# Performance work log

Measured on AMD Instinct MI355X. Metric: run time of the kernel, lower is better.

The kernel has to match this reference:

```python
import jax, jax.numpy as jnp
import numpy as np

NUM_EXPERTS = 4


def _conv1x1(w, b, x):
    # w: [out,in], b: [out], x: [B,in,H,W]
    return jnp.einsum('oc,bchw->bohw', w, x) + b[None, :, None, None]


def _sobel(x):
    c = x.shape[1]
    kx = jnp.array([[-1., 0., 1.], [-2., 0., 2.], [-1., 0., 1.]], dtype=x.dtype)
    ky = jnp.array([[-1., -2., -1.], [0., 0., 0.], [1., 2., 1.]], dtype=x.dtype)
    wx = jnp.broadcast_to(kx[None, None], (c, 1, 3, 3))
    wy = jnp.broadcast_to(ky[None, None], (c, 1, 3, 3))
    dn = ('NCHW', 'OIHW', 'NCHW')
    gx = jax.lax.conv_general_dilated(x, wx, (1, 1), [(1, 1), (1, 1)],
                                      dimension_numbers=dn, feature_group_count=c)
    gy = jax.lax.conv_general_dilated(x, wy, (1, 1), [(1, 1), (1, 1)],
                                      dimension_numbers=dn, feature_group_count=c)
    return gx, gy


def _bilinear_sample(x, gx, gy):
    # torch F.grid_sample(mode='bilinear', padding_mode='zeros', align_corners=False)
    # x: [B,C,H,W]; gx, gy: [B,Hs,Ws] normalized coords in [-1,1]
    B, C, H, W = x.shape
    ix = ((gx + 1.0) * W - 1.0) * 0.5
    iy = ((gy + 1.0) * H - 1.0) * 0.5
    x0 = jnp.floor(ix)
    y0 = jnp.floor(iy)
    wx1 = ix - x0
    wx0 = 1.0 - wx1
    wy1 = iy - y0
    wy0 = 1.0 - wy1
    xf = x.reshape(B, C, H * W)

    def gather(xc, yc):
        valid = (xc >= 0) & (xc <= W - 1) & (yc >= 0) & (yc <= H - 1)
        xi = jnp.clip(xc, 0, W - 1).astype(jnp.int32)
        yi = jnp.clip(yc, 0, H - 1).astype(jnp.int32)
        idx = yi * W + xi  # [B,Hs,Ws]
        v = jax.vmap(lambda xb, ib: xb[:, ib])(xf, idx)  # [B,C,Hs,Ws]
        return v * valid[:, None].astype(x.dtype)

    return (gather(x0, y0) * (wx0 * wy0)[:, None]
            + gather(x0 + 1, y0) * (wx1 * wy0)[:, None]
            + gather(x0, y0 + 1) * (wx0 * wy1)[:, None]
            + gather(x0 + 1, y0 + 1) * (wx1 * wy1)[:, None])


def _forward(x, wc_e, we_e, wb1, bb1, wb2, bb2, wr, br, wo, bo, wcv, bcv, scale, scale2):
    B, c, h, w = x.shape
    sh = round(h * scale)
    sw = round(w * scale2)

    grad_x, grad_y = _sobel(x)

    # relative-offset coordinate embedding, [1,4,sh,sw]
    ih = (jnp.arange(sh, dtype=x.dtype) + 0.5) / scale
    coor_h = ih - jnp.floor(ih + 0.001) - 0.5  # [sh]
    iw = (jnp.arange(sw, dtype=x.dtype) + 0.5) / scale2
    coor_w = iw - jnp.floor(iw + 0.001) - 0.5  # [sw]
    inp = jnp.stack([
        jnp.full((sh, sw), 1.0 / scale2, dtype=x.dtype),
        jnp.full((sh, sw), 1.0 / scale, dtype=x.dtype),
        jnp.broadcast_to(coor_h[:, None], (sh, sw)),
        jnp.broadcast_to(coor_w[None, :], (sh, sw)),
    ], axis=0)[None]

    emb = jax.nn.relu(_conv1x1(wb2, bb2, jax.nn.relu(_conv1x1(wb1, bb1, inp))))
    offset = _conv1x1(wo, bo, emb)                 # [1,2,sh,sw]
    routing = jax.nn.sigmoid(_conv1x1(wr, br, emb))  # [1,E,sh,sw]

    # per-pixel soft mixture of expert compress/expand matrices
    rw = routing.reshape(NUM_EXPERTS, sh * sw).T   # [N,E]
    wc = (rw @ wc_e.reshape(NUM_EXPERTS, -1)).reshape(sh, sw, c // 8, c)
    we = (rw @ we_e.reshape(NUM_EXPERTS, -1)).reshape(sh, sw, c, c // 8)

    feat = _conv1x1(wcv, bcv, jnp.concatenate([x, grad_x, grad_y], axis=1))  # [B,64,h,w]

    # base grid (align_corners=True-style normalization, as in the source) + learned offsets
    gx0 = ((jnp.arange(sw, dtype=x.dtype) + 0.5) / scale2 - 0.5) * 2.0 / (w - 1) - 1.0
    gy0 = ((jnp.arange(sh, dtype=x.dtype) + 0.5) / scale - 0.5) * 2.0 / (h - 1) - 1.0
    gx = jnp.broadcast_to(gx0[None, None, :] + offset[:, 0] * (2.0 / (w - 1)), (B, sh, sw))
    gy = jnp.broadcast_to(gy0[None, :, None] + offset[:, 1] * (2.0 / (h - 1)), (B, sh, sw))

    fea0 = _bilinear_sample(feat, gx, gy)          # [B,64,sh,sw]

    mid = jnp.einsum('hwkc,bchw->bhwk', wc, fea0)  # per-pixel compress (k=C//8)
    out = jnp.einsum('hwck,bhwk->bchw', we, mid)   # per-pixel expand
    return out + fea0


def setup_inputs() -> dict:
    key = jax.random.key(0)
    ks = jax.random.split(key, 13)
    s = 0.05
    return {
        'x': jax.random.normal(ks[0], (2, 64, 192, 192), jnp.float32),
        'weight_compress': jax.random.normal(ks[1], (4, 8, 64), jnp.float32) * s,
        'weight_expand': jax.random.normal(ks[2], (4, 64, 8), jnp.float32) * s,
        'w_body1': jax.random.normal(ks[3], (64, 4), jnp.float32) * s,
        'b_body1': jax.random.normal(ks[4], (64,), jnp.float32) * s,
        'w_body2': jax.random.normal(ks[5], (64, 64), jnp.float32) * s,
        'b_body2': jax.random.normal(ks[6], (64,), jnp.float32) * s,
        'w_routing': jax.random.normal(ks[7], (4, 64), jnp.float32) * s,
        'b_routing': jax.random.normal(ks[8], (4,), jnp.float32) * s,
        'w_offset': jax.random.normal(ks[9], (2, 64), jnp.float32) * s,
        'b_offset': jax.random.normal(ks[10], (2,), jnp.float32) * s,
        'w_conv': jax.random.normal(ks[11], (64, 192), jnp.float32) * s,
        'b_conv': jax.random.normal(ks[12], (64,), jnp.float32) * s,
        'scale': 2,
        'scale2': 2,
    }


def reference(x, weight_compress, weight_expand, w_body1, b_body1, w_body2, b_body2,
              w_routing, b_routing, w_offset, b_offset, w_conv, b_conv, scale, scale2):
    return _forward(x, weight_compress, weight_expand, w_body1, b_body1, w_body2, b_body2,
                    w_routing, b_routing, w_offset, b_offset, w_conv, b_conv, scale, scale2)
```

## Files before the change

### kernel.cpp

```cpp
#include <hip/hip_runtime.h>
#include <hip/hip_bf16.h>
#include <math.h>

#define BN  2
#define CN  64
#define HN  192
#define WN  192
#define SH  384
#define SW  384
#define HW  (HN * WN)
#define NPIX (BN * HN * WN)

typedef __attribute__((ext_vector_type(8))) short bf16x8;
typedef __attribute__((ext_vector_type(4))) float f32x4;

#define KPAD 200

__device__ inline unsigned short f2bf(float f) {
    unsigned int u = __float_as_uint(f);
    u += 0x7fffu + ((u >> 16) & 1u);
    return (unsigned short)(u >> 16);
}

__device__ inline void sobel_col(const float* __restrict__ xc,
    size_t oT, size_t oM, size_t oB, int j, int jL, int jR,
    float mt, float mb, float mLt, float mLm, float mLb,
    float mRt, float mRm, float mRb, bool isL, bool isR,
    float& m_out, float& sx, float& sy)
{
    float t   = xc[oT + j] * mt;
    float m   = xc[oM + j];
    float btm = xc[oB + j] * mb;
    float hLt = xc[oT + jL] * mLt;
    float hLm = xc[oM + jL] * mLm;
    float hLb = xc[oB + jL] * mLb;
    float hRt = xc[oT + jR] * mRt;
    float hRm = xc[oM + jR] * mRm;
    float hRb = xc[oB + jR] * mRb;
    float tl  = __shfl_up(t, 1),   ml_ = __shfl_up(m, 1),   bl_ = __shfl_up(btm, 1);
    float tr  = __shfl_down(t, 1), mr_ = __shfl_down(m, 1), br_ = __shfl_down(btm, 1);
    float n0 = isL ? hLt : tl;
    float n3 = isL ? hLm : ml_;
    float n6 = isL ? hLb : bl_;
    float n2 = isR ? hRt : tr;
    float n5 = isR ? hRm : mr_;
    float n8 = isR ? hRb : br_;
    m_out = m;
    sx = (n2 - n0) + 2.f * (n5 - n3) + (n8 - n6);
    sy = (n6 - n0) + 2.f * (btm - t) + (n8 - n2);
}

__global__ __launch_bounds__(256) void feat_kernel(
    const float* __restrict__ x,
    const float* __restrict__ wcv,
    const float* __restrict__ bcv,
    float* __restrict__ feat)
{
    __shared__ unsigned short Bs[64 * KPAD];

    int bi = blockIdx.x;
    int jt = bi % 3;
    int t2 = bi / 3;
    int i  = t2 % HN;
    int b  = t2 / HN;
    int j0 = jt * 64;

    int tid  = threadIdx.x;
    int w    = __builtin_amdgcn_readfirstlane(tid >> 6);
    int lane = tid & 63;

    int mrow = (w << 4) + (lane & 15);
    int kb   = (lane >> 4) << 3;
    bf16x8 afrag[6];
    {
        const float* wr_ = wcv + mrow * 192 + kb;
#pragma unroll
        for (int ks = 0; ks < 6; ++ks) {
            float4 lo = *(const float4*)(wr_ + ks * 32);
            float4 hi = *(const float4*)(wr_ + ks * 32 + 4);
            bf16x8 a;
            a[0] = (short)f2bf(lo.x); a[1] = (short)f2bf(lo.y);
            a[2] = (short)f2bf(lo.z); a[3] = (short)f2bf(lo.w);
            a[4] = (short)f2bf(hi.x); a[5] = (short)f2bf(hi.y);
            a[6] = (short)f2bf(hi.z); a[7] = (short)f2bf(hi.w);
            afrag[ks] = a;
        }
    }

    bool ok_t = (i > 0), ok_b = (i < HN - 1);
    bool okL = (j0 > 0), okR = (j0 + 64 < WN);
    float mt = ok_t ? 1.f : 0.f, mb = ok_b ? 1.f : 0.f;
    int rT = ok_t ? i - 1 : i;
    int rB = ok_b ? i + 1 : i;
    int jL = okL ? j0 - 1 : j0;
    int jR = okR ? j0 + 64 : j0;
    float mLt = okL ? mt : 0.f, mLm = okL ? 1.f : 0.f, mLb = okL ? mb : 0.f;
    float mRt = okR ? mt : 0.f, mRm = okR ? 1.f : 0.f, mRb = okR ? mb : 0.f;
    bool isL = (lane == 0), isR = (lane == 63);

    const float* xb = x + (size_t)b * CN * HW;
    size_t oT = (size_t)rT * WN, oM = (size_t)i * WN, oB = (size_t)rB * WN;
    int j = j0 + lane;

    unsigned short* brow = Bs + lane * KPAD;
#pragma unroll 2
    for (int cp = 0; cp < 8; ++cp) {
        int c0 = (w << 4) + (cp << 1);
        float m0, sx0, sy0, m1, sx1, sy1;
        sobel_col(xb + (size_t)c0 * HW, oT, oM, oB, j, jL, jR,
                  mt, mb, mLt, mLm, mLb, mRt, mRm, mRb, isL, isR, m0, sx0, sy0);
        sobel_col(xb + (size_t)(c0 + 1) * HW, oT, oM, oB, j, jL, jR,
                  mt, mb, mLt, mLm, mLb, mRt, mRm, mRb, isL, isR, m1, sx1, sy1);
        *(unsigned int*)(brow + c0)       = (unsigned int)f2bf(m0)  | ((unsigned int)f2bf(m1)  << 16);
        *(unsigned int*)(brow + 64 + c0)  = (unsigned int)f2bf(sx0) | ((unsigned int)f2bf(sx1) << 16);
        *(unsigned int*)(brow + 128 + c0) = (unsigned int)f2bf(sy0) | ((unsigned int)f2bf(sy1) << 16);
    }

    __syncthreads();

    f32x4 acc[4] = {};
    const unsigned short* bp = Bs + (lane & 15) * KPAD + ((lane >> 4) << 3);
#pragma unroll
    for (int nt = 0; nt < 4; ++nt) {
        const unsigned short* bnt = bp + nt * 16 * KPAD;
#pragma unroll
        for (int ks = 0; ks < 6; ++ks) {
            bf16x8 bf = *(const bf16x8*)(bnt + ks * 32);
            acc[nt] = __builtin_amdgcn_mfma_f32_16x16x32_bf16(afrag[ks], bf, acc[nt], 0, 0, 0);
        }
    }

    int n0 = j0 + (lane & 15);
    int mbase = (w << 4) + ((lane >> 4) << 2);
    size_t outb = (size_t)b * CN * HW + (size_t)i * WN;
#pragma unroll
    for (int rr = 0; rr < 4; ++rr) {
        int m = mbase + rr;
        float bias = bcv[m];
        size_t rowb = outb + (size_t)m * HW + n0;
#pragma unroll
        for (int nt = 0; nt < 4; ++nt)
            feat[rowb + nt * 16] = acc[nt][rr] + bias;
    }
}

__device__ inline void run_mlp(int lane, float in0, float in1, float chv, float cwv,
    const float* __restrict__ wb1, const float* __restrict__ bb1,
    const float* __restrict__ wb2, const float* __restrict__ bb2,
    const float* __restrict__ wr,  const float* __restrict__ wo, float p[6])
{
    float4 w1 = ((const float4*)wb1)[lane];
    float h1 = fmaxf(bb1[lane] + w1.x * in0 + w1.y * in1 + w1.z * chv + w1.w * cwv, 0.f);
    const float4* w2row = (const float4*)(wb2 + lane * 64);
    float acc = bb2[lane];
#pragma unroll
    for (int q = 0; q < 16; ++q) {
        float4 wv = w2row[q];
        acc += wv.x * __shfl(h1, q * 4 + 0)
             + wv.y * __shfl(h1, q * 4 + 1)
             + wv.z * __shfl(h1, q * 4 + 2)
             + wv.w * __shfl(h1, q * 4 + 3);
    }
    float h2 = fmaxf(acc, 0.f);
#pragma unroll
    for (int e = 0; e < 4; ++e) p[e] = wr[e * 64 + lane] * h2;
#pragma unroll
    for (int e = 0; e < 2; ++e) p[4 + e] = wo[e * 64 + lane] * h2;
#pragma unroll
    for (int m = 1; m < 64; m <<= 1) {
#pragma unroll
        for (int e = 0; e < 6; ++e) p[e] += __shfl_xor(p[e], m);
    }
}

__global__ __launch_bounds__(256) void mlp_table_kernel(
    const float* __restrict__ wb1, const float* __restrict__ bb1,
    const float* __restrict__ wb2, const float* __restrict__ bb2,
    const float* __restrict__ wr,  const float* __restrict__ br,
    const float* __restrict__ wo,  const float* __restrict__ bo,
    const float* __restrict__ wce, const float* __restrict__ wee,
    const int* __restrict__ scale_p, const int* __restrict__ scale2_p,
    float* __restrict__ tblEntry, float* __restrict__ tblMix)
{
    int sc = scale_p[0], sc2 = scale2_p[0];
    int w = (blockIdx.x * 256 + threadIdx.x) >> 6;
    int lane = threadIdx.x & 63;
    float scale = (float)sc, scale2 = (float)sc2;
    float in0 = 1.f / scale2, in1 = 1.f / scale;
    bool fast = (sc2 == 2 && sc <= 16);

    if (fast) {
        if (w >= sc) return;
        int pi = w;
        float ih = (pi + 0.5f) / scale;
        float chv = ih - floorf(ih + 0.001f) - 0.5f;
        float p0[6], p1[6];
        {
            float iw = 0.5f / scale2;
            float cwv = iw - floorf(iw + 0.001f) - 0.5f;
            run_mlp(lane, in0, in1, chv, cwv, wb1, bb1, wb2, bb2, wr, wo, p0);
        }
        {
            float iw = 1.5f / scale2;
            float cwv = iw - floorf(iw + 0.001f) - 0.5f;
            run_mlp(lane, in0, in1, chv, cwv, wb1, bb1, wb2, bb2, wr, wo, p1);
        }
        float reE[4], reO[4];
#pragma unroll
        for (int e = 0; e < 4; ++e) {
            reE[e] = 1.f / (1.f + expf(-(p0[e] + br[e])));
            reO[e] = 1.f / (1.f + expf(-(p1[e] + br[e])));
        }
        if (lane == 0) {
            float* t0 = tblEntry + (pi * 2 + 0) * 8;
            float* t1 = tblEntry + (pi * 2 + 1) * 8;
#pragma unroll
            for (int e = 0; e < 4; ++e) { t0[e] = reE[e]; t1[e] = reO[e]; }
            t0[4] = p0[4] + bo[0]; t0[5] = p0[5] + bo[1];
            t1[4] = p1[4] + bo[0]; t1[5] = p1[5] + bo[1];
        }
        float* mp = tblMix + pi * 2048;
        for (int idx = lane; idx < 512; idx += 64) {
            float cE = reE[0] * wce[idx]        + reE[1] * wce[512 + idx]
                     + reE[2] * wce[1024 + idx] + reE[3] * wce[1536 + idx];
            float cO = reO[0] * wce[idx]        + reO[1] * wce[512 + idx]
                     + reO[2] * wce[1024 + idx] + reO[3] * wce[1536 + idx];
            mp[idx]       = 0.5f * (cE + cO);
            mp[512 + idx] = 0.5f * (cE - cO);
            float eE = reE[0] * wee[idx]        + reE[1] * wee[512 + idx]
                     + reE[2] * wee[1024 + idx] + reE[3] * wee[1536 + idx];
            float eO = reO[0] * wee[idx]        + reO[1] * wee[512 + idx]
                     + reO[2] * wee[1024 + idx] + reO[3] * wee[1536 + idx];
            mp[1024 + idx] = 0.5f * (eE + eO);
            mp[1536 + idx] = 0.5f * (eE - eO);
        }
    } else {
        if (w >= sc * sc2) return;
        int pi = w / sc2, pj = w - pi * sc2;
        float ih = (pi + 0.5f) / scale;
        float chv = ih - floorf(ih + 0.001f) - 0.5f;
        float iw = (pj + 0.5f) / scale2;
        float cwv = iw - floorf(iw + 0.001f) - 0.5f;
        float p[6];
        run_mlp(lane, in0, in1, chv, cwv, wb1, bb1, wb2, bb2, wr, wo, p);
        if (lane == 0) {
            float* tp = tblEntry + w * 8;
#pragma unroll
            for (int e = 0; e < 4; ++e) tp[e] = 1.f / (1.f + expf(-(p[e] + br[e])));
            tp[4] = p[4] + bo[0];
            tp[5] = p[5] + bo[1];
        }
    }
}

__global__ __launch_bounds__(256) void out_kernel(
    const float* __restrict__ feat,
    const float* __restrict__ tblEntry,
    const float* __restrict__ tblMix,
    const float* __restrict__ wce,
    const float* __restrict__ wee,
    const int* __restrict__ scale_p, const int* __restrict__ scale2_p,
    float* __restrict__ out)
{
    __shared__ float midp[4 * 64 * 9];

    int Bk = blockIdx.x;
    int T = gridDim.x;
    int t = ((T & 7) == 0) ? ((Bk & 7) * (T >> 3) + (Bk >> 3)) : Bk;

    int tid = threadIdx.x;
    int g = __builtin_amdgcn_readfirstlane(tid >> 6);
    int lane = tid & 63;
    int pix0 = t * 64;
    int b = pix0 / (SH * SW);
    int r0 = pix0 - b * SH * SW;
    int i = r0 / SW;
    int j0 = r0 - i * SW;
    int j = j0 + lane;
    int r = r0 + lane;

    int sc = scale_p[0], sc2 = scale2_p[0];
    float scale = (float)sc, scale2 = (float)sc2;
    int pi = i - (i / sc) * sc;
    int pj = j - (j / sc2) * sc2;
    int entry = pi * sc2 + pj;
    float offx = tblEntry[entry * 8 + 4];
    float offy = tblEntry[entry * 8 + 5];

    const float inv_wm1 = 2.f / (float)(WN - 1);
    const float inv_hm1 = 2.f / (float)(HN - 1);
    float gx = ((j + 0.5f) / scale2 - 0.5f) * inv_wm1 - 1.f + offx * inv_wm1;
    float gy = ((i + 0.5f) / scale  - 0.5f) * inv_hm1 - 1.f + offy * inv_hm1;

    float ix = ((gx + 1.f) * WN - 1.f) * 0.5f;
    float iy = ((gy + 1.f) * HN - 1.f) * 0.5f;
    float fx0 = floorf(ix), fy0 = floorf(iy);
    int x0 = (int)fx0, y0 = (int)fy0;
    float wx1 = ix - fx0, wx0 = 1.f - wx1;
    float wy1 = iy - fy0, wy0 = 1.f - wy1;

    bool vx0 = (x0 >= 0) && (x0 <= WN - 1);
    bool vx1 = (x0 + 1 >= 0) && (x0 + 1 <= WN - 1);
    bool vy0 = (y0 >= 0) && (y0 <= HN - 1);
    bool vy1 = (y0 + 1 >= 0) && (y0 + 1 <= HN - 1);
    bool v00 = vx0 && vy0, v10 = vx1 && vy0, v01 = vx0 && vy1, v11 = vx1 && vy1;
    float w00 = wx0 * wy0, w10 = wx1 * wy0, w01 = wx0 * wy1, w11 = wx1 * wy1;

    int i00 = y0 * WN + x0;
    int i10 = i00 + 1;
    int i01 = i00 + WN;
    int i11 = i01 + 1;

    const float* fb = feat + (size_t)b * CN * HW;

    float f0[16];
#pragma unroll
    for (int cc = 0; cc < 16; ++cc) {
        const float* fc = fb + (size_t)(g * 16 + cc) * HW;
        float a  = v00 ? fc[i00] : 0.f;
        float bq = v10 ? fc[i10] : 0.f;
        float cq = v01 ? fc[i01] : 0.f;
        float dq = v11 ? fc[i11] : 0.f;
        f0[cc] = a * w00 + bq * w10 + cq * w01 + dq * w11;
    }

    bool fast = (sc2 == 2 && sc <= 16);
    if (fast) {
        float sgn = (pj == 0) ? 1.f : -1.f;
        const float* mp = tblMix + pi * 2048;
#pragma unroll
        for (int k = 0; k < 8; ++k) {
            const float* wa = mp + k * 64 + g * 16;
            const float* wd = mp + 512 + k * 64 + g * 16;
            float dA = 0.f, dB = 0.f;
#pragma unroll
            for (int cc = 0; cc < 16; ++cc) { dA += wa[cc] * f0[cc]; dB += wd[cc] * f0[cc]; }
            midp[(g * 64 + lane) * 9 + k] = fmaf(sgn, dB, dA);
        }
        __syncthreads();
        float mid[8];
#pragma unroll
        for (int k = 0; k < 8; ++k)
            mid[k] = midp[(0 * 64 + lane) * 9 + k] + midp[(1 * 64 + lane) * 9 + k]
                   + midp[(2 * 64 + lane) * 9 + k] + midp[(3 * 64 + lane) * 9 + k];
#pragma unroll
        for (int cc = 0; cc < 16; ++cc) {
            int c = g * 16 + cc;
            const float* wa = mp + 1024 + c * 8;
            const float* wd = mp + 1536 + c * 8;
            float vA = 0.f, vB = 0.f;
#pragma unroll
            for (int k = 0; k < 8; ++k) { vA += wa[k] * mid[k]; vB += wd[k] * mid[k]; }
            out[(size_t)(b * CN + c) * SH * SW + r] = f0[cc] + fmaf(sgn, vB, vA);
        }
    } else {
        float4 rw = *(const float4*)(tblEntry + entry * 8);
        float re[4] = {rw.x, rw.y, rw.z, rw.w};
        float part[4][8];
#pragma unroll
        for (int e = 0; e < 4; ++e) {
#pragma unroll
            for (int k = 0; k < 8; ++k) {
                const float* wrow = wce + (e * 8 + k) * 64 + g * 16;
                float d = 0.f;
#pragma unroll
                for (int cc = 0; cc < 16; ++cc) d += wrow[cc] * f0[cc];
                part[e][k] = d;
            }
        }
#pragma unroll
        for (int k = 0; k < 8; ++k) {
            float m = re[0] * part[0][k] + re[1] * part[1][k]
                    + re[2] * part[2][k] + re[3] * part[3][k];
            midp[(g * 64 + lane) * 9 + k] = m;
        }
        __syncthreads();
        float mid[8];
#pragma unroll
        for (int k = 0; k < 8; ++k)
            mid[k] = midp[(0 * 64 + lane) * 9 + k] + midp[(1 * 64 + lane) * 9 + k]
                   + midp[(2 * 64 + lane) * 9 + k] + midp[(3 * 64 + lane) * 9 + k];
#pragma unroll
        for (int cc = 0; cc < 16; ++cc) {
            int c = g * 16 + cc;
            float v = f0[cc];
#pragma unroll
            for (int e = 0; e < 4; ++e) {
                const float* wrow = wee + (e * 64 + c) * 8;
                float d = 0.f;
#pragma unroll
                for (int k = 0; k < 8; ++k) d += wrow[k] * mid[k];
                v += re[e] * d;
            }
            out[(size_t)(b * CN + c) * SH * SW + r] = v;
        }
    }
}

extern "C" void kernel_launch(void* const* d_in, const int* in_sizes, int n_in,
                              void* d_out, int out_size, void* d_ws, size_t ws_size,
                              hipStream_t stream) {
    const float* x    = (const float*)d_in[0];
    const float* wce  = (const float*)d_in[1];
    const float* wee  = (const float*)d_in[2];
    const float* wb1  = (const float*)d_in[3];
    const float* bb1  = (const float*)d_in[4];
    const float* wb2  = (const float*)d_in[5];
    const float* bb2  = (const float*)d_in[6];
    const float* wr   = (const float*)d_in[7];
    const float* br   = (const float*)d_in[8];
    const float* wo   = (const float*)d_in[9];
    const float* bo   = (const float*)d_in[10];
    const float* wcv  = (const float*)d_in[11];
    const float* bcv  = (const float*)d_in[12];
    const int*   scale  = (const int*)d_in[13];
    const int*   scale2 = (const int*)d_in[14];
    float* out = (float*)d_out;

    float* feat     = (float*)d_ws;
    float* tblEntry = feat + (size_t)BN * CN * HW;
    float* tblMix   = tblEntry + 256 * 8;

    feat_kernel<<<BN * HN * 3, 256, 0, stream>>>(x, wcv, bcv, feat);
    mlp_table_kernel<<<64, 256, 0, stream>>>(wb1, bb1, wb2, bb2, wr, br, wo, bo,
                                             wce, wee, scale, scale2,
                                             tblEntry, tblMix);
    out_kernel<<<BN * SH * SW / 64, 256, 0, stream>>>(feat, tblEntry, tblMix,
                                                      wce, wee, scale, scale2, out);
}
```

Before: 169.8 us.

## Fold compress/expand into 64x64 bf16 matrix and apply via MFMA

The table kernel now multiplies the expert-mixed compress (8x64) and expand (64x8) weights into a full 64x64 per-row matrix, split into even and odd column halves and stored as bf16. The output kernel stages the bilinear features in shared memory as fp32 and bf16, then runs the 64x64 channel mixing with 16x16x32 bf16 MFMA instructions instead of the two scalar fp32 dot-product stages and their shared-memory reduction. This trades more FLOPs (a rank-8 product expanded to a dense 64x64) and bf16 rounding for matrix-core throughput and fewer syncs. Output stores keep per-pixel rows, with the sign picked from pixel parity.

```diff
diff --git a/kernel.cpp b/kernel.cpp
--- a/kernel.cpp
+++ b/kernel.cpp
@@ -180,61 +180,85 @@
     const float* __restrict__ wo,  const float* __restrict__ bo,
     const float* __restrict__ wce, const float* __restrict__ wee,
     const int* __restrict__ scale_p, const int* __restrict__ scale2_p,
-    float* __restrict__ tblEntry, float* __restrict__ tblMix)
+    float* __restrict__ tblEntry, unsigned short* __restrict__ tblM)
 {
+    __shared__ float reL[8];
+    __shared__ float wcmL[2 * 512];
+    __shared__ float wemL[2 * 512];
+
     int sc = scale_p[0], sc2 = scale2_p[0];
-    int w = (blockIdx.x * 256 + threadIdx.x) >> 6;
-    int lane = threadIdx.x & 63;
+    int tid = threadIdx.x;
+    int lane = tid & 63;
     float scale = (float)sc, scale2 = (float)sc2;
     float in0 = 1.f / scale2, in1 = 1.f / scale;
     bool fast = (sc2 == 2 && sc <= 16);
 
     if (fast) {
-        if (w >= sc) return;
-        int pi = w;
-        float ih = (pi + 0.5f) / scale;
-        float chv = ih - floorf(ih + 0.001f) - 0.5f;
-        float p0[6], p1[6];
-        {
-            float iw = 0.5f / scale2;
-            float cwv = iw - floorf(iw + 0.001f) - 0.5f;
-            run_mlp(lane, in0, in1, chv, cwv, wb1, bb1, wb2, bb2, wr, wo, p0);
-        }
-        {
-            float iw = 1.5f / scale2;
-            float cwv = iw - floorf(iw + 0.001f) - 0.5f;
-            run_mlp(lane, in0, in1, chv, cwv, wb1, bb1, wb2, bb2, wr, wo, p1);
-        }
-        float reE[4], reO[4];
-#pragma unroll
-        for (int e = 0; e < 4; ++e) {
-            reE[e] = 1.f / (1.f + expf(-(p0[e] + br[e])));
-            reO[e] = 1.f / (1.f + expf(-(p1[e] + br[e])));
-        }
-        if (lane == 0) {
-            float* t0 = tblEntry + (pi * 2 + 0) * 8;
-            float* t1 = tblEntry + (pi * 2 + 1) * 8;
-#pragma unroll
-            for (int e = 0; e < 4; ++e) { t0[e] = reE[e]; t1[e] = reO[e]; }
-            t0[4] = p0[4] + bo[0]; t0[5] = p0[5] + bo[1];
-            t1[4] = p1[4] + bo[0]; t1[5] = p1[5] + bo[1];
-        }
-        float* mp = tblMix + pi * 2048;
-        for (int idx = lane; idx < 512; idx += 64) {
-            float cE = reE[0] * wce[idx]        + reE[1] * wce[512 + idx]
-                     + reE[2] * wce[1024 + idx] + reE[3] * wce[1536 + idx];
-            float cO = reO[0] * wce[idx]        + reO[1] * wce[512 + idx]
-                     + reO[2] * wce[1024 + idx] + reO[3] * wce[1536 + idx];
-            mp[idx]       = 0.5f * (cE + cO);
-            mp[512 + idx] = 0.5f * (cE - cO);
-            float eE = reE[0] * wee[idx]        + reE[1] * wee[512 + idx]
-                     + reE[2] * wee[1024 + idx] + reE[3] * wee[1536 + idx];
-            float eO = reO[0] * wee[idx]        + reO[1] * wee[512 + idx]
-                     + reO[2] * wee[1024 + idx] + reO[3] * wee[1536 + idx];
-            mp[1024 + idx] = 0.5f * (eE + eO);
-            mp[1536 + idx] = 0.5f * (eE - eO);
+        int pi = blockIdx.x;
+        if (pi >= sc) return;
+        if (tid < 64) {
+            float ih = (pi + 0.5f) / scale;
+            float chv = ih - floorf(ih + 0.001f) - 0.5f;
+            float p0[6], p1[6];
+            {
+                float iw = 0.5f / scale2;
+                float cwv = iw - floorf(iw + 0.001f) - 0.5f;
+                run_mlp(lane, in0, in1, chv, cwv, wb1, bb1, wb2, bb2, wr, wo, p0);
+            }
+            {
+                float iw = 1.5f / scale2;
+                float cwv = iw - floorf(iw + 0.001f) - 0.5f;
+                run_mlp(lane, in0, in1, chv, cwv, wb1, bb1, wb2, bb2, wr, wo, p1);
+            }
+            if (lane == 0) {
+                float* t0 = tblEntry + (pi * 2 + 0) * 8;
+                float* t1 = tblEntry + (pi * 2 + 1) * 8;
+#pragma unroll
+                for (int e = 0; e < 4; ++e) {
+                    float rE = 1.f / (1.f + expf(-(p0[e] + br[e])));
+                    float rO = 1.f / (1.f + expf(-(p1[e] + br[e])));
+                    t0[e] = rE; t1[e] = rO;
+                    reL[e] = rE; reL[4 + e] = rO;
+                }
+                t0[4] = p0[4] + bo[0]; t0[5] = p0[5] + bo[1];
+                t1[4] = p1[4] + bo[0]; t1[5] = p1[5] + bo[1];
+            }
+        }
+        __syncthreads();
+        float reE0 = reL[0], reE1 = reL[1], reE2 = reL[2], reE3 = reL[3];
+        float reO0 = reL[4], reO1 = reL[5], reO2 = reL[6], reO3 = reL[7];
+        for (int idx = tid; idx < 512; idx += 256) {
+            float a = wce[idx], bq = wce[512 + idx], c = wce[1024 + idx], d = wce[1536 + idx];
+            wcmL[idx]       = reE0 * a + reE1 * bq + reE2 * c + reE3 * d;
+            wcmL[512 + idx] = reO0 * a + reO1 * bq + reO2 * c + reO3 * d;
+            float e_ = wee[idx], f = wee[512 + idx], g = wee[1024 + idx], h = wee[1536 + idx];
+            wemL[idx]       = reE0 * e_ + reE1 * f + reE2 * g + reE3 * h;
+            wemL[512 + idx] = reO0 * e_ + reO1 * f + reO2 * g + reO3 * h;
+        }
+        __syncthreads();
+        int co  = tid >> 2;
+        int ci0 = (tid & 3) << 4;
+        float w0[8], w1[8];
+#pragma unroll
+        for (int k = 0; k < 8; ++k) {
+            w0[k] = wemL[co * 8 + k];
+            w1[k] = wemL[512 + co * 8 + k];
+        }
+        unsigned short* tb = tblM + (size_t)pi * 2 * 4096;
+#pragma unroll
+        for (int cc = 0; cc < 16; ++cc) {
+            int ci = ci0 + cc;
+            float m0 = 0.f, m1 = 0.f;
+#pragma unroll
+            for (int k = 0; k < 8; ++k) {
+                m0 += w0[k] * wcmL[k * 64 + ci];
+                m1 += w1[k] * wcmL[512 + k * 64 + ci];
+            }
+            tb[co * 64 + ci]        = f2bf(0.5f * (m0 + m1));
+            tb[4096 + co * 64 + ci] = f2bf(0.5f * (m0 - m1));
         }
     } else {
+        int w = (blockIdx.x * 256 + threadIdx.x) >> 6;
         if (w >= sc * sc2) return;
         int pi = w / sc2, pj = w - pi * sc2;
         float ih = (pi + 0.5f) / scale;
@@ -253,16 +277,20 @@
     }
 }
 
+#define BKP 72
 __global__ __launch_bounds__(256) void out_kernel(
     const float* __restrict__ feat,
     const float* __restrict__ tblEntry,
-    const float* __restrict__ tblMix,
+    const unsigned short* __restrict__ tblM,
     const float* __restrict__ wce,
     const float* __restrict__ wee,
     const int* __restrict__ scale_p, const int* __restrict__ scale2_p,
     float* __restrict__ out)
 {
-    __shared__ float midp[4 * 64 * 9];
+    __shared__ __attribute__((aligned(16))) float smem[64 * 65 + 64 * (BKP / 2)];
+    float* fea32 = smem;
+    unsigned short* Bsv = (unsigned short*)(smem + 64 * 65);
+    float* midp = smem;
 
     int Bk = blockIdx.x;
     int T = gridDim.x;
@@ -326,32 +354,52 @@
 
     bool fast = (sc2 == 2 && sc <= 16);
     if (fast) {
-        float sgn = (pj == 0) ? 1.f : -1.f;
-        const float* mp = tblMix + pi * 2048;
-#pragma unroll
-        for (int k = 0; k < 8; ++k) {
-            const float* wa = mp + k * 64 + g * 16;
-            const float* wd = mp + 512 + k * 64 + g * 16;
-            float dA = 0.f, dB = 0.f;
-#pragma unroll
-            for (int cc = 0; cc < 16; ++cc) { dA += wa[cc] * f0[cc]; dB += wd[cc] * f0[cc]; }
-            midp[(g * 64 + lane) * 9 + k] = fmaf(sgn, dB, dA);
-        }
+        int px = lane;
+#pragma unroll
+        for (int cc = 0; cc < 16; ++cc)
+            fea32[px * 65 + g * 16 + cc] = f0[cc];
+#pragma unroll
+        for (int cc = 0; cc < 16; cc += 2) {
+            unsigned int pk = (unsigned int)f2bf(f0[cc]) | ((unsigned int)f2bf(f0[cc + 1]) << 16);
+            *(unsigned int*)(Bsv + px * BKP + g * 16 + cc) = pk;
+        }
+
+        int row = lane & 15;
+        int kb  = (lane >> 4) << 3;
+        const unsigned short* Mb = tblM + (size_t)pi * 2 * 4096 + (g * 16 + row) * 64 + kb;
+        bf16x8 a1[2], a2[2];
+        a1[0] = *(const bf16x8*)(Mb);
+        a1[1] = *(const bf16x8*)(Mb + 32);
+        a2[0] = *(const bf16x8*)(Mb + 4096);
+        a2[1] = *(const bf16x8*)(Mb + 4096 + 32);
+
         __syncthreads();
-        float mid[8];
-#pragma unroll
-        for (int k = 0; k < 8; ++k)
-            mid[k] = midp[(0 * 64 + lane) * 9 + k] + midp[(1 * 64 + lane) * 9 + k]
-                   + midp[(2 * 64 + lane) * 9 + k] + midp[(3 * 64 + lane) * 9 + k];
-#pragma unroll
-        for (int cc = 0; cc < 16; ++cc) {
-            int c = g * 16 + cc;
-            const float* wa = mp + 1024 + c * 8;
-            const float* wd = mp + 1536 + c * 8;
-            float vA = 0.f, vB = 0.f;
-#pragma unroll
-            for (int k = 0; k < 8; ++k) { vA += wa[k] * mid[k]; vB += wd[k] * mid[k]; }
-            out[(size_t)(b * CN + c) * SH * SW + r] = f0[cc] + fmaf(sgn, vB, vA);
+
+        f32x4 acc1[4] = {}, acc2[4] = {};
+        const unsigned short* bp = Bsv + (lane & 15) * BKP + kb;
+#pragma unroll
+        for (int nt = 0; nt < 4; ++nt) {
+            const unsigned short* bnt = bp + nt * 16 * BKP;
+#pragma unroll
+            for (int ks = 0; ks < 2; ++ks) {
+                bf16x8 bf = *(const bf16x8*)(bnt + ks * 32);
+                acc1[nt] = __builtin_amdgcn_mfma_f32_16x16x32_bf16(a1[ks], bf, acc1[nt], 0, 0, 0);
+                acc2[nt] = __builtin_amdgcn_mfma_f32_16x16x32_bf16(a2[ks], bf, acc2[nt], 0, 0, 0);
+            }
+        }
+
+        int q = lane >> 4;
+#pragma unroll
+        for (int rr = 0; rr < 4; ++rr) {
+            int c = g * 16 + q * 4 + rr;
+            size_t rowb = (size_t)(b * CN + c) * SH * SW + r0;
+#pragma unroll
+            for (int nt = 0; nt < 4; ++nt) {
+                int n = (lane & 15) + nt * 16;
+                float sgn = (n & 1) ? -1.f : 1.f;
+                float v = fea32[n * 65 + c] + acc1[nt][rr] + sgn * acc2[nt][rr];
+                out[rowb + n] = v;
+            }
         }
     } else {
         float4 rw = *(const float4*)(tblEntry + entry * 8);
@@ -419,12 +467,12 @@
 
     float* feat     = (float*)d_ws;
     float* tblEntry = feat + (size_t)BN * CN * HW;
-    float* tblMix   = tblEntry + 256 * 8;
+    unsigned short* tblM = (unsigned short*)(tblEntry + 256 * 8);
 
     feat_kernel<<<BN * HN * 3, 256, 0, stream>>>(x, wcv, bcv, feat);
     mlp_table_kernel<<<64, 256, 0, stream>>>(wb1, bb1, wb2, bb2, wr, br, wo, bo,
                                              wce, wee, scale, scale2,
-                                             tblEntry, tblMix);
-    out_kernel<<<BN * SH * SW / 64, 256, 0, stream>>>(feat, tblEntry, tblMix,
+                                             tblEntry, tblM);
+    out_kernel<<<BN * SH * SW / 64, 256, 0, stream>>>(feat, tblEntry, tblM,
                                                       wce, wee, scale, scale2, out);
 }
```

After: 162.2 us. 4.5% less time.
